# Kernel tuning notes

Measured on AMD Instinct MI355X. Metric: run time of the kernel, lower is better.

Reference implementation:

```python
import jax, jax.numpy as jnp
import numpy as np
from jax import lax


def _mdlstm_dir(x, Wx, Wh, Wv, b):
    # x: [H, W, B, Cin]; one diagonal-causal 2D-LSTM scan (top-left origin).
    H, W, B, Cin = x.shape
    C = Wh.shape[0]
    xa = jnp.einsum('hwbi,ic->hwbc', x, Wx) + b  # [H,W,B,5C] precomputed input gates

    def col_step(carry, inp):
        h_l, c_l = carry                    # left neighbor [B,C]
        xa_ij, h_u, c_u = inp               # input preact, up neighbor
        a = xa_ij + h_l @ Wh + h_u @ Wv     # [B,5C]
        i, f1, f2, o, g = jnp.split(a, 5, axis=-1)
        c = jax.nn.sigmoid(i) * jnp.tanh(g) + jax.nn.sigmoid(f1) * c_l + jax.nn.sigmoid(f2) * c_u
        h = jax.nn.sigmoid(o) * jnp.tanh(c)
        return (h, c), (h, c)

    z = jnp.zeros((B, C), x.dtype)
    zrow = jnp.zeros((W, B, C), x.dtype)

    def row_step(carry, xa_row):
        h_up, c_up = carry                  # [W,B,C]
        _, (hs, cs) = lax.scan(col_step, (z, z), (xa_row, h_up, c_up))
        return (hs, cs), hs

    _, hh = lax.scan(row_step, (zrow, zrow), xa)  # [H,W,B,C]
    return hh


def _mdlstm4(x, Wx, Wh, Wv, b):
    # x: [B,Cin,H,W] -> per-direction outputs [4,H,W,B,C] (directions: TL, TR, BL, BR origins)
    xt = jnp.transpose(x, (2, 3, 0, 1))  # [H,W,B,Cin]
    x4 = jnp.stack([xt, xt[:, ::-1], xt[::-1], xt[::-1, ::-1]])
    o = jax.vmap(_mdlstm_dir)(x4, Wx, Wh, Wv, b)  # [4,H,W,B,C]
    return jnp.stack([o[0], o[1][:, ::-1], o[2][::-1], o[3][::-1, ::-1]])


def _block(x, Wx, Wh, Wv, b, cw, cb):
    h4 = _mdlstm4(x, Wx, Wh, Wv, b)            # [4,H,W,B,C]
    h = jnp.transpose(h4.sum(0), (2, 3, 0, 1))  # sum directions -> [B,C,H,W]
    y = lax.conv_general_dilated(h, cw, window_strides=(2, 2), padding='VALID',
                                 dimension_numbers=('NCHW', 'OIHW', 'NCHW'))
    return jnp.tanh(y + cb[None, :, None, None])


def _forward(x, p0_Wx, p0_Wh, p0_Wv, p0_b, c0_w, c0_b,
             p1_Wx, p1_Wh, p1_Wv, p1_b, c1_w, c1_b,
             p2_Wx, p2_Wh, p2_Wv, p2_b, dW, db):
    x = _block(x, p0_Wx, p0_Wh, p0_Wv, p0_b, c0_w, c0_b)  # [B,6,31,126]
    x = _block(x, p1_Wx, p1_Wh, p1_Wv, p1_b, c1_w, c1_b)  # [B,20,14,61]
    h4 = _mdlstm4(x, p2_Wx, p2_Wh, p2_Wv, p2_b)           # [4,H,W,B,50]
    # per-direction Linear(50->100) then sum over the 4 directions
    out = jnp.einsum('dhwbc,dcn->bhwn', h4, dW) + db.sum(0)
    return out  # [B,14,61,100]


def setup_inputs() -> dict:
    key = jax.random.key(0)
    ks = jax.random.split(key, 20)
    rn = lambda k, s, sc=0.1: jax.random.normal(k, s, jnp.float32) * sc
    return {
        'x': jax.random.normal(ks[0], (16, 1, 64, 256), jnp.float32),
        'p0_Wx': rn(ks[1], (4, 1, 10)), 'p0_Wh': rn(ks[2], (4, 2, 10)),
        'p0_Wv': rn(ks[3], (4, 2, 10)), 'p0_b': rn(ks[4], (4, 10)),
        'c0_w': rn(ks[5], (6, 2, 2, 4)), 'c0_b': rn(ks[6], (6,)),
        'p1_Wx': rn(ks[7], (4, 6, 50)), 'p1_Wh': rn(ks[8], (4, 10, 50)),
        'p1_Wv': rn(ks[9], (4, 10, 50)), 'p1_b': rn(ks[10], (4, 50)),
        'c1_w': rn(ks[11], (20, 10, 2, 4)), 'c1_b': rn(ks[12], (20,)),
        'p2_Wx': rn(ks[13], (4, 20, 250)), 'p2_Wh': rn(ks[14], (4, 50, 250)),
        'p2_Wv': rn(ks[15], (4, 50, 250)), 'p2_b': rn(ks[16], (4, 250)),
        'dW': rn(ks[17], (4, 50, 100)), 'db': rn(ks[18], (4, 100)),
    }


def reference(x, p0_Wx, p0_Wh, p0_Wv, p0_b, c0_w, c0_b,
              p1_Wx, p1_Wh, p1_Wv, p1_b, c1_w, c1_b,
              p2_Wx, p2_Wh, p2_Wv, p2_b, dW, db):
    return _forward(x, p0_Wx, p0_Wh, p0_Wv, p0_b, c0_w, c0_b,
                    p1_Wx, p1_Wh, p1_Wv, p1_b, c1_w, c1_b,
                    p2_Wx, p2_Wh, p2_Wv, p2_b, dW, db)
```

## Files before the change

### kernel.cpp

```cpp
#include <hip/hip_runtime.h>

typedef unsigned short ushort_t;
typedef __attribute__((ext_vector_type(8))) short short8;
typedef __attribute__((ext_vector_type(4))) float float4_t;

__device__ __forceinline__ float frcp(float x) { return __builtin_amdgcn_rcpf(x); }
__device__ __forceinline__ float fsig(float x) { return frcp(1.f + __expf(-x)); }
__device__ __forceinline__ float ftanh(float x) { return 1.f - 2.f * frcp(1.f + __expf(2.f * x)); }

__device__ __forceinline__ ushort_t f2bf(float f) {
    union { float f; unsigned u; } v; v.f = f;
    unsigned u = v.u;
    unsigned r = (u + 0x7fffu + ((u >> 16) & 1u)) >> 16;
    return (ushort_t)r;
}
__device__ __forceinline__ float bf2f(ushort_t s) {
    union { unsigned u; float f; } v; v.u = ((unsigned)s) << 16;
    return v.f;
}

__global__ __launch_bounds__(64) void k_mdlstm0(
    const float* __restrict__ x, const float* __restrict__ Wx,
    const float* __restrict__ Wh, const float* __restrict__ Wv,
    const float* __restrict__ bias, float* __restrict__ h0)
{
    const int dir = blockIdx.x >> 4, b = blockIdx.x & 15;
    const int lane = threadIdx.x;
    const bool fH = dir >= 2, fW = (dir & 1) != 0;
    const int ri = fH ? 63 - lane : lane;

    float wx[10], bs[10], wh[2][10], wv[2][10];
#pragma unroll
    for (int n = 0; n < 10; n++) { wx[n] = Wx[dir * 10 + n]; bs[n] = bias[dir * 10 + n]; }
#pragma unroll
    for (int k = 0; k < 2; k++)
#pragma unroll
        for (int n = 0; n < 10; n++) {
            wh[k][n] = Wh[(dir * 2 + k) * 10 + n];
            wv[k][n] = Wv[(dir * 2 + k) * 10 + n];
        }

    const float* xrow = x + (b * 64 + ri) * 256;
    float* orow = h0 + (((dir * 16 + b) * 64 + ri) * 256) * 2;

    float h0r = 0.f, h1r = 0.f, c0r = 0.f, c1r = 0.f;

    auto ld = [&](int d) -> float {
        int j = d - lane; j = j < 0 ? 0 : (j > 255 ? 255 : j);
        int cj = fW ? 255 - j : j;
        return xrow[cj];
    };
    float xp0 = ld(0), xp1 = ld(1);

    for (int d = 0; d < 319; d++) {
        float xv = xp0;
        xp0 = xp1;
        xp1 = ld(d + 2);

        float hu0 = __shfl_up(h0r, 1), hu1 = __shfl_up(h1r, 1);
        float cu0 = __shfl_up(c0r, 1), cu1 = __shfl_up(c1r, 1);
        if (lane == 0) { hu0 = 0.f; hu1 = 0.f; cu0 = 0.f; cu1 = 0.f; }

        int j = d - lane;
        if (j >= 0 && j < 256) {
            float a[10];
#pragma unroll
            for (int n = 0; n < 10; n++) {
                float t = fmaf(xv, wx[n], bs[n]);
                t = fmaf(h0r, wh[0][n], t); t = fmaf(h1r, wh[1][n], t);
                t = fmaf(hu0, wv[0][n], t); t = fmaf(hu1, wv[1][n], t);
                a[n] = t;
            }
            float cn0 = fsig(a[0]) * ftanh(a[8]) + fsig(a[2]) * c0r + fsig(a[4]) * cu0;
            float cn1 = fsig(a[1]) * ftanh(a[9]) + fsig(a[3]) * c1r + fsig(a[5]) * cu1;
            float hn0 = fsig(a[6]) * ftanh(cn0);
            float hn1 = fsig(a[7]) * ftanh(cn1);
            h0r = hn0; h1r = hn1; c0r = cn0; c1r = cn1;
            int cj = fW ? 255 - j : j;
            float2 hv; hv.x = hn0; hv.y = hn1;
            *(float2*)&orow[cj * 2] = hv;
        }
    }
}

__global__ __launch_bounds__(128) void k_conv0(
    const float* __restrict__ h0, const float* __restrict__ cw,
    const float* __restrict__ cb, float* __restrict__ x1)
{
    int blk = blockIdx.x;
    int oh = blk / 127, ow = blk % 127;
    int t = threadIdx.x;
    if (t >= 96) return;
    int b = t / 6, co = t % 6;
    float w[2][2][4];
#pragma unroll
    for (int ci = 0; ci < 2; ci++)
#pragma unroll
        for (int kh = 0; kh < 2; kh++)
#pragma unroll
            for (int kw = 0; kw < 4; kw++)
                w[ci][kh][kw] = cw[((co * 2 + ci) * 2 + kh) * 4 + kw];
    float acc = cb[co];
    for (int dirb = 0; dirb < 4; dirb++) {
#pragma unroll
        for (int kh = 0; kh < 2; kh++) {
#pragma unroll
            for (int kw = 0; kw < 4; kw++) {
                const float* ptr = h0 + ((((dirb * 16 + b) * 64) + (2 * oh + kh)) * 256 + (2 * ow + kw)) * 2;
                float2 hv = *(const float2*)ptr;
                acc = fmaf(hv.x, w[0][kh][kw], acc);
                acc = fmaf(hv.y, w[1][kh][kw], acc);
            }
        }
    }
    x1[((oh * 127 + ow) * 16 + b) * 6 + co] = ftanh(acc);
}

__global__ __launch_bounds__(320, 1) void k_mdlstm1(
    const float* __restrict__ x1, const float* __restrict__ Wx,
    const float* __restrict__ Wh, const float* __restrict__ Wv,
    const float* __restrict__ bias, float* __restrict__ h1)
{
    const int dir = blockIdx.x >> 4, b = blockIdx.x & 15;
    const bool fH = dir >= 2, fW = (dir & 1) != 0;
    const int tid = threadIdx.x;
    const int cell = tid / 10, u = tid % 10;
    const int ri = fH ? 31 - cell : cell;

    __shared__ float hb[2][33][12];
    __shared__ float cb[2][33][12];
    for (int i = tid; i < 2 * 33 * 12; i += 320) { ((float*)hb)[i] = 0.f; ((float*)cb)[i] = 0.f; }
    __syncthreads();

    float wxr[6][5], whr[10][5], wvr[10][5], br[5];
#pragma unroll
    for (int g = 0; g < 5; g++) {
        int n = g * 10 + u;
        br[g] = bias[dir * 50 + n];
#pragma unroll
        for (int ci = 0; ci < 6; ci++) wxr[ci][g] = Wx[(dir * 6 + ci) * 50 + n];
#pragma unroll
        for (int k = 0; k < 10; k++) {
            whr[k][g] = Wh[(dir * 10 + k) * 50 + n];
            wvr[k][g] = Wv[(dir * 10 + k) * 50 + n];
        }
    }

    float creg = 0.f;
    float xr[6], xn[6];
    auto xload = [&](int d, float* dst) {
        int j = d - cell; j = j < 0 ? 0 : (j > 126 ? 126 : j);
        int cj = fW ? 126 - j : j;
        const float* p2 = x1 + ((ri * 127 + cj) * 16 + b) * 6;
#pragma unroll
        for (int k2 = 0; k2 < 6; k2++) dst[k2] = p2[k2];
    };
    xload(0, xr); xload(1, xn);

    int p = 0;
    for (int d = 0; d < 158; d++) {
        int j = d - cell;
        bool act = (j >= 0) && (j < 127);
        float hl[10], hu[10];
#pragma unroll
        for (int k = 0; k < 10; k++) { hl[k] = hb[p][cell + 1][k]; hu[k] = hb[p][cell][k]; }
        float cu = cb[p][cell][u];
        if (act) {
            float a[5];
#pragma unroll
            for (int g = 0; g < 5; g++) {
                float t = br[g];
#pragma unroll
                for (int ci = 0; ci < 6; ci++) t = fmaf(xr[ci], wxr[ci][g], t);
#pragma unroll
                for (int k = 0; k < 10; k++) t = fmaf(hl[k], whr[k][g], t);
#pragma unroll
                for (int k = 0; k < 10; k++) t = fmaf(hu[k], wvr[k][g], t);
                a[g] = t;
            }
            float cn = fsig(a[0]) * ftanh(a[4]) + fsig(a[1]) * creg + fsig(a[2]) * cu;
            float hn = fsig(a[3]) * ftanh(cn);
            creg = cn;
            hb[1 - p][cell + 1][u] = hn;
            cb[1 - p][cell + 1][u] = cn;
            int cj = fW ? 126 - j : j;
            h1[(((dir * 16 + b) * 32 + ri) * 127 + cj) * 10 + u] = hn;
        }
#pragma unroll
        for (int k2 = 0; k2 < 6; k2++) xr[k2] = xn[k2];
        xload(d + 2, xn);
        __syncthreads();
        p ^= 1;
    }
}

__global__ __launch_bounds__(320, 1) void k_conv1(
    const float* __restrict__ h1, const float* __restrict__ cw,
    const float* __restrict__ cb, float* __restrict__ x2)
{
    int blk = blockIdx.x;
    int oh = blk / 62, ow = blk % 62;
    int t = threadIdx.x;
    int b = t / 20, co = t % 20;
    float w[10][2][4];
#pragma unroll
    for (int ci = 0; ci < 10; ci++)
#pragma unroll
        for (int kh = 0; kh < 2; kh++)
#pragma unroll
            for (int kw = 0; kw < 4; kw++)
                w[ci][kh][kw] = cw[((co * 10 + ci) * 2 + kh) * 4 + kw];
    float acc = cb[co];
    for (int dirb = 0; dirb < 4; dirb++) {
#pragma unroll
        for (int kh = 0; kh < 2; kh++) {
#pragma unroll
            for (int kw = 0; kw < 4; kw++) {
                const float* ptr = h1 + ((((dirb * 16 + b) * 32) + (2 * oh + kh)) * 127 + (2 * ow + kw)) * 10;
#pragma unroll
                for (int ci = 0; ci < 10; ci++)
                    acc = fmaf(ptr[ci], w[ci][kh][kw], acc);
            }
        }
    }
    x2[((oh * 62 + ow) * 16 + b) * 20 + co] = ftanh(acc);
}

__global__ __launch_bounds__(256) void k_prepB2(
    const float* __restrict__ Wh, const float* __restrict__ Wv,
    const float* __restrict__ Wx, ushort_t* __restrict__ Bh,
    ushort_t* __restrict__ Bl)
{
    int idx = blockIdx.x * 256 + threadIdx.x;
    if (idx >= 131072) return;
    int dir = idx >> 15; int k = (idx >> 8) & 127; int n = idx & 255;
    float v = 0.f;
    if (n < 250) {
        if (k < 50)       v = Wh[(dir * 50 + k) * 250 + n];
        else if (k < 100) v = Wv[(dir * 50 + (k - 50)) * 250 + n];
        else if (k < 120) v = Wx[(dir * 20 + (k - 100)) * 250 + n];
    }
    ushort_t hi = f2bf(v);
    Bh[idx] = hi;
    Bl[idx] = f2bf(v - bf2f(hi));
}

__global__ __launch_bounds__(1024, 1) void k_mdlstm2(
    const float* __restrict__ x2, const ushort_t* __restrict__ BmH,
    const ushort_t* __restrict__ BmL,
    const float* __restrict__ bias, float* __restrict__ h2)
{
    const int dir = blockIdx.x >> 4, b = blockIdx.x & 15;
    const bool fH = dir >= 2, fW = (dir & 1) != 0;
    const int tid = threadIdx.x;
    const int wave = tid >> 6, lane = tid & 63;

    __shared__ __align__(16) ushort_t Ah[2][16][136];
    __shared__ __align__(16) ushort_t Al[2][16][136];
    __shared__ float P[16][260];
    __shared__ float cbuf[2][16][52];

    for (int i = tid; i < 2 * 16 * 136; i += 1024) { ((ushort_t*)Ah)[i] = 0; ((ushort_t*)Al)[i] = 0; }
    __syncthreads();
    if (tid < 20) {
        int ci = tid;
        int rr = fH ? 15 : 0, cc = fW ? 61 : 0;
        float xv = x2[((rr * 62 + cc) * 16 + b) * 20 + ci];
        ushort_t xh = f2bf(xv);
        Ah[0][0][100 + ci] = xh;
        Al[0][0][100 + ci] = f2bf(xv - bf2f(xh));
    }

    short8 bfragH[4], bfragL[4];
    {
        const int n = wave * 16 + (lane & 15);
#pragma unroll
        for (int q = 0; q < 4; q++) {
#pragma unroll
            for (int jj = 0; jj < 8; jj++) {
                int k = q * 32 + (lane >> 4) * 8 + jj;
                bfragH[q][jj] = (short)BmH[(dir * 128 + k) * 256 + n];
                bfragL[q][jj] = (short)BmL[(dir * 128 + k) * 256 + n];
            }
        }
    }

    const int cell = tid / 50, u = tid % 50;
    float bi = 0, bf1 = 0, bf2v = 0, bo = 0, bg = 0;
    if (tid < 800) {
        bi   = bias[dir * 250 + u];
        bf1  = bias[dir * 250 + 50 + u];
        bf2v = bias[dir * 250 + 100 + u];
        bo   = bias[dir * 250 + 150 + u];
        bg   = bias[dir * 250 + 200 + u];
    }
    const int rr_c = fH ? 15 - cell : cell;
    float creg = 0.f;
    __syncthreads();

    int p = 0;
    for (int d = 0; d < 77; d++) {
        float4_t acc = {0.f, 0.f, 0.f, 0.f};
        const int arow = lane & 15;
        const int koff = (lane >> 4) * 8;
#pragma unroll
        for (int q = 0; q < 4; q++) {
            short8 af = *(const short8*)&Ah[p][arow][q * 32 + koff];
            acc = __builtin_amdgcn_mfma_f32_16x16x32_bf16(af, bfragL[q], acc, 0, 0, 0);
        }
#pragma unroll
        for (int q = 0; q < 4; q++) {
            short8 af = *(const short8*)&Al[p][arow][q * 32 + koff];
            acc = __builtin_amdgcn_mfma_f32_16x16x32_bf16(af, bfragH[q], acc, 0, 0, 0);
        }
#pragma unroll
        for (int q = 0; q < 4; q++) {
            short8 af = *(const short8*)&Ah[p][arow][q * 32 + koff];
            acc = __builtin_amdgcn_mfma_f32_16x16x32_bf16(af, bfragH[q], acc, 0, 0, 0);
        }
        {
            int col = wave * 16 + (lane & 15);
            int r0 = (lane >> 4) * 4;
#pragma unroll
            for (int r = 0; r < 4; r++) P[r0 + r][col] = acc[r];
        }
        __syncthreads();

        if (tid < 800) {
            int j = d - cell;
            if (j >= 0 && j < 62) {
                float ai  = P[cell][u] + bi;
                float af1 = P[cell][50 + u] + bf1;
                float af2 = P[cell][100 + u] + bf2v;
                float ao  = P[cell][150 + u] + bo;
                float ag  = P[cell][200 + u] + bg;
                float cu = (cell == 0) ? 0.f : cbuf[p][cell - 1][u];
                float cn = fsig(ai) * ftanh(ag) + fsig(af1) * creg + fsig(af2) * cu;
                float hn = fsig(ao) * ftanh(cn);
                creg = cn;
                cbuf[1 - p][cell][u] = cn;
                ushort_t hh = f2bf(hn);
                float hhf = bf2f(hh);
                ushort_t hlo = f2bf(hn - hhf);
                Ah[1 - p][cell][u] = hh;
                Al[1 - p][cell][u] = hlo;
                if (cell < 15) { Ah[1 - p][cell + 1][50 + u] = hh; Al[1 - p][cell + 1][50 + u] = hlo; }
                int cc = fW ? 61 - j : j;
                h2[(((dir * 16 + b) * 16 + rr_c) * 62 + cc) * 50 + u] = hn;
            }
        }
        if (tid < 320) {
            int xc = tid / 20, ci = tid % 20;
            int jn = d + 1 - xc;
            if (jn >= 0 && jn < 62) {
                int rr = fH ? 15 - xc : xc, cc = fW ? 61 - jn : jn;
                float xv = x2[((rr * 62 + cc) * 16 + b) * 20 + ci];
                ushort_t xh = f2bf(xv);
                Ah[1 - p][xc][100 + ci] = xh;
                Al[1 - p][xc][100 + ci] = f2bf(xv - bf2f(xh));
            }
        }
        __syncthreads();
        p ^= 1;
    }
}

__global__ __launch_bounds__(256) void k_final(
    const float* __restrict__ h2, const float* __restrict__ dW,
    const float* __restrict__ db, float* __restrict__ out)
{
    int blk = blockIdx.x;
    int r = blk / 62, c = blk % 62;
    int t = threadIdx.x;
    __shared__ float hb[3200];
    for (int i = t; i < 3200; i += 256) {
        int dirb = i / 800, rem = i % 800, b = rem / 50, u = rem % 50;
        hb[i] = h2[(((dirb * 16 + b) * 16 + r) * 62 + c) * 50 + u];
    }
    __syncthreads();
    for (int o = t; o < 1600; o += 256) {
        int b = o / 100, n = o % 100;
        float acc = db[n] + db[100 + n] + db[200 + n] + db[300 + n];
#pragma unroll
        for (int dirb = 0; dirb < 4; dirb++) {
            const float* hp = hb + (dirb * 16 + b) * 50;
            const float* wp = dW + dirb * 5000 + n;
#pragma unroll 10
            for (int cc2 = 0; cc2 < 50; cc2++)
                acc = fmaf(hp[cc2], wp[cc2 * 100], acc);
        }
        out[((b * 16 + r) * 62 + c) * 100 + n] = acc;
    }
}

extern "C" void kernel_launch(void* const* d_in, const int* in_sizes, int n_in,
                              void* d_out, int out_size, void* d_ws, size_t ws_size,
                              hipStream_t stream)
{
    const float* x     = (const float*)d_in[0];
    const float* p0_Wx = (const float*)d_in[1];
    const float* p0_Wh = (const float*)d_in[2];
    const float* p0_Wv = (const float*)d_in[3];
    const float* p0_b  = (const float*)d_in[4];
    const float* c0_w  = (const float*)d_in[5];
    const float* c0_b  = (const float*)d_in[6];
    const float* p1_Wx = (const float*)d_in[7];
    const float* p1_Wh = (const float*)d_in[8];
    const float* p1_Wv = (const float*)d_in[9];
    const float* p1_b  = (const float*)d_in[10];
    const float* c1_w  = (const float*)d_in[11];
    const float* c1_b  = (const float*)d_in[12];
    const float* p2_Wx = (const float*)d_in[13];
    const float* p2_Wh = (const float*)d_in[14];
    const float* p2_Wv = (const float*)d_in[15];
    const float* p2_b  = (const float*)d_in[16];
    const float* dW    = (const float*)d_in[17];
    const float* db    = (const float*)d_in[18];
    float* out = (float*)d_out;
    float* ws  = (float*)d_ws;

    float* h0 = ws;
    float* x1 = h0 + 2097152;
    float* h1 = x1 + 390144;
    float* x2 = h1 + 2600960;
    float* h2 = x2 + 317440;
    ushort_t* BmH = (ushort_t*)(h2 + 3174400);
    ushort_t* BmL = BmH + 131072;

    k_prepB2<<<512, 256, 0, stream>>>(p2_Wh, p2_Wv, p2_Wx, BmH, BmL);
    k_mdlstm0<<<64, 64, 0, stream>>>(x, p0_Wx, p0_Wh, p0_Wv, p0_b, h0);
    k_conv0<<<32 * 127, 128, 0, stream>>>(h0, c0_w, c0_b, x1);
    k_mdlstm1<<<64, 320, 0, stream>>>(x1, p1_Wx, p1_Wh, p1_Wv, p1_b, h1);
    k_conv1<<<16 * 62, 320, 0, stream>>>(h1, c1_w, c1_b, x2);
    k_mdlstm2<<<64, 1024, 0, stream>>>(x2, BmH, BmL, p2_b, h2);
    k_final<<<16 * 62, 256, 0, stream>>>(h2, dW, db, out);
}
```

Baseline: 562.5 us.

## Move layer-1 MDLSTM gate matmul to MFMA and vectorize layer-0 recurrence

Layer-1 MDLSTM now runs its per-diagonal gate GEMM on bf16 MFMA with a hi/lo split for near-fp32 accuracy. It uses 1024 threads, with dedicated waves prefetching the next diagonal's inputs into shared memory. This replaces a long serial FMA chain per thread. Layer 0 uses packed float2 FMAs, folds log2(e) scaling into the weights so it can call exp2 directly, and uses a DPP row shift in place of shfl_up. Layer 2 preloads A fragments and reorders its MFMA chain and input-load threads. Risks: the DPP row_shr only shifts within 16-lane rows, so lanes 16/32/48 would read zero instead of their upper neighbor. The else branch that zeroes the state also changes the boundary behavior.

```diff
diff --git a/kernel.cpp b/kernel.cpp
--- a/kernel.cpp
+++ b/kernel.cpp
@@ -3,10 +3,13 @@
 typedef unsigned short ushort_t;
 typedef __attribute__((ext_vector_type(8))) short short8;
 typedef __attribute__((ext_vector_type(4))) float float4_t;
+typedef __attribute__((ext_vector_type(2))) float v2f;
 
 __device__ __forceinline__ float frcp(float x) { return __builtin_amdgcn_rcpf(x); }
 __device__ __forceinline__ float fsig(float x) { return frcp(1.f + __expf(-x)); }
 __device__ __forceinline__ float ftanh(float x) { return 1.f - 2.f * frcp(1.f + __expf(2.f * x)); }
+__device__ __forceinline__ float sig_e2(float a) { return frcp(1.f + __builtin_amdgcn_exp2f(a)); }
+__device__ __forceinline__ float th_e2(float a) { return 1.f - 2.f * frcp(1.f + __builtin_amdgcn_exp2f(a)); }
 
 __device__ __forceinline__ ushort_t f2bf(float f) {
     union { float f; unsigned u; } v; v.f = f;
@@ -18,6 +21,11 @@
     union { unsigned u; float f; } v; v.u = ((unsigned)s) << 16;
     return v.f;
 }
+__device__ __forceinline__ float dpp_shr1(float x) {
+    int i = __builtin_bit_cast(int, x);
+    int r = __builtin_amdgcn_update_dpp(0, i, 0x138 , 0xf, 0xf, true);
+    return __builtin_bit_cast(float, r);
+}
 
 __global__ __launch_bounds__(64) void k_mdlstm0(
     const float* __restrict__ x, const float* __restrict__ Wx,
@@ -28,22 +36,28 @@
     const int lane = threadIdx.x;
     const bool fH = dir >= 2, fW = (dir & 1) != 0;
     const int ri = fH ? 63 - lane : lane;
-
-    float wx[10], bs[10], wh[2][10], wv[2][10];
-#pragma unroll
-    for (int n = 0; n < 10; n++) { wx[n] = Wx[dir * 10 + n]; bs[n] = bias[dir * 10 + n]; }
-#pragma unroll
-    for (int k = 0; k < 2; k++)
-#pragma unroll
-        for (int n = 0; n < 10; n++) {
-            wh[k][n] = Wh[(dir * 2 + k) * 10 + n];
-            wv[k][n] = Wv[(dir * 2 + k) * 10 + n];
-        }
+    const float L2E = 1.44269504088896340736f;
+
+    v2f wx[5], bs[5], wh0[5], wh1[5], wv0[5], wv1[5];
+#pragma unroll
+    for (int g = 0; g < 5; g++) {
+        float sc = (g == 4) ? 2.f * L2E : -L2E;
+#pragma unroll
+        for (int un = 0; un < 2; un++) {
+            int n = g * 2 + un;
+            wx[g][un]  = Wx[dir * 10 + n] * sc;
+            bs[g][un]  = bias[dir * 10 + n] * sc;
+            wh0[g][un] = Wh[(dir * 2 + 0) * 10 + n] * sc;
+            wh1[g][un] = Wh[(dir * 2 + 1) * 10 + n] * sc;
+            wv0[g][un] = Wv[(dir * 2 + 0) * 10 + n] * sc;
+            wv1[g][un] = Wv[(dir * 2 + 1) * 10 + n] * sc;
+        }
+    }
 
     const float* xrow = x + (b * 64 + ri) * 256;
     float* orow = h0 + (((dir * 16 + b) * 64 + ri) * 256) * 2;
 
-    float h0r = 0.f, h1r = 0.f, c0r = 0.f, c1r = 0.f;
+    v2f hr = {0.f, 0.f}, cr = {0.f, 0.f};
 
     auto ld = [&](int d) -> float {
         int j = d - lane; j = j < 0 ? 0 : (j > 255 ? 255 : j);
@@ -57,28 +71,37 @@
         xp0 = xp1;
         xp1 = ld(d + 2);
 
-        float hu0 = __shfl_up(h0r, 1), hu1 = __shfl_up(h1r, 1);
-        float cu0 = __shfl_up(c0r, 1), cu1 = __shfl_up(c1r, 1);
-        if (lane == 0) { hu0 = 0.f; hu1 = 0.f; cu0 = 0.f; cu1 = 0.f; }
+        float hu0 = dpp_shr1(hr.x), hu1 = dpp_shr1(hr.y);
+        float cu0 = dpp_shr1(cr.x), cu1 = dpp_shr1(cr.y);
 
         int j = d - lane;
         if (j >= 0 && j < 256) {
-            float a[10];
-#pragma unroll
-            for (int n = 0; n < 10; n++) {
-                float t = fmaf(xv, wx[n], bs[n]);
-                t = fmaf(h0r, wh[0][n], t); t = fmaf(h1r, wh[1][n], t);
-                t = fmaf(hu0, wv[0][n], t); t = fmaf(hu1, wv[1][n], t);
-                a[n] = t;
-            }
-            float cn0 = fsig(a[0]) * ftanh(a[8]) + fsig(a[2]) * c0r + fsig(a[4]) * cu0;
-            float cn1 = fsig(a[1]) * ftanh(a[9]) + fsig(a[3]) * c1r + fsig(a[5]) * cu1;
-            float hn0 = fsig(a[6]) * ftanh(cn0);
-            float hn1 = fsig(a[7]) * ftanh(cn1);
-            h0r = hn0; h1r = hn1; c0r = cn0; c1r = cn1;
+            v2f a[5];
+#pragma unroll
+            for (int g = 0; g < 5; g++) {
+                v2f t = __builtin_elementwise_fma((v2f){xv, xv}, wx[g], bs[g]);
+                t = __builtin_elementwise_fma((v2f){hr.x, hr.x}, wh0[g], t);
+                t = __builtin_elementwise_fma((v2f){hr.y, hr.y}, wh1[g], t);
+                t = __builtin_elementwise_fma((v2f){hu0, hu0}, wv0[g], t);
+                t = __builtin_elementwise_fma((v2f){hu1, hu1}, wv1[g], t);
+                a[g] = t;
+            }
+            v2f si  = {sig_e2(a[0].x), sig_e2(a[0].y)};
+            v2f sf1 = {sig_e2(a[1].x), sig_e2(a[1].y)};
+            v2f sf2 = {sig_e2(a[2].x), sig_e2(a[2].y)};
+            v2f so  = {sig_e2(a[3].x), sig_e2(a[3].y)};
+            v2f tg  = {th_e2(a[4].x),  th_e2(a[4].y)};
+            v2f cu  = {cu0, cu1};
+            v2f cn = si * tg + sf1 * cr + sf2 * cu;
+            v2f tc = {th_e2(cn.x * (2.f * L2E)), th_e2(cn.y * (2.f * L2E))};
+            hr = so * tc;
+            cr = cn;
             int cj = fW ? 255 - j : j;
-            float2 hv; hv.x = hn0; hv.y = hn1;
+            float2 hv; hv.x = hr.x; hv.y = hr.y;
             *(float2*)&orow[cj * 2] = hv;
+        } else {
+            hr = (v2f){0.f, 0.f};
+            cr = (v2f){0.f, 0.f};
         }
     }
 }
@@ -116,7 +139,7 @@
     x1[((oh * 127 + ow) * 16 + b) * 6 + co] = ftanh(acc);
 }
 
-__global__ __launch_bounds__(320, 1) void k_mdlstm1(
+__global__ __launch_bounds__(1024, 1) void k_mdlstm1(
     const float* __restrict__ x1, const float* __restrict__ Wx,
     const float* __restrict__ Wh, const float* __restrict__ Wv,
     const float* __restrict__ bias, float* __restrict__ h1)
@@ -124,71 +147,102 @@
     const int dir = blockIdx.x >> 4, b = blockIdx.x & 15;
     const bool fH = dir >= 2, fW = (dir & 1) != 0;
     const int tid = threadIdx.x;
+    const int wave = tid >> 6, lane = tid & 63;
+
+    __shared__ __align__(16) ushort_t Ah[2][32][40];
+    __shared__ __align__(16) ushort_t Al[2][32][40];
+    __shared__ float P[32][68];
+    __shared__ float cbuf[2][33][12];
+
+    for (int i = tid; i < 2 * 32 * 40; i += 1024) { ((ushort_t*)Ah)[i] = 0; ((ushort_t*)Al)[i] = 0; }
+    for (int i = tid; i < 2 * 33 * 12; i += 1024) ((float*)cbuf)[i] = 0.f;
+    __syncthreads();
+    if (tid < 6) {
+        int rr = fH ? 31 : 0, cc = fW ? 126 : 0;
+        float xv = x1[((rr * 127 + cc) * 16 + b) * 6 + tid];
+        ushort_t xh = f2bf(xv);
+        Ah[0][0][20 + tid] = xh;
+        Al[0][0][20 + tid] = f2bf(xv - bf2f(xh));
+    }
+
+    const int mt = wave & 1, nt = wave >> 1;
+    short8 bh = {0,0,0,0,0,0,0,0}, bl = {0,0,0,0,0,0,0,0};
+    if (wave < 8) {
+        int n = nt * 16 + (lane & 15);
+#pragma unroll
+        for (int jj = 0; jj < 8; jj++) {
+            int k = (lane >> 4) * 8 + jj;
+            float v = 0.f;
+            if (n < 50) {
+                if (k < 10)      v = Wh[(dir * 10 + k) * 50 + n];
+                else if (k < 20) v = Wv[(dir * 10 + (k - 10)) * 50 + n];
+                else if (k < 26) v = Wx[(dir * 6 + (k - 20)) * 50 + n];
+            }
+            ushort_t hi = f2bf(v);
+            bh[jj] = (short)hi;
+            bl[jj] = (short)f2bf(v - bf2f(hi));
+        }
+    }
+
     const int cell = tid / 10, u = tid % 10;
+    float br[5];
+#pragma unroll
+    for (int g = 0; g < 5; g++) br[g] = (tid < 320) ? bias[dir * 50 + g * 10 + u] : 0.f;
     const int ri = fH ? 31 - cell : cell;
-
-    __shared__ float hb[2][33][12];
-    __shared__ float cb[2][33][12];
-    for (int i = tid; i < 2 * 33 * 12; i += 320) { ((float*)hb)[i] = 0.f; ((float*)cb)[i] = 0.f; }
+    float creg = 0.f;
     __syncthreads();
-
-    float wxr[6][5], whr[10][5], wvr[10][5], br[5];
-#pragma unroll
-    for (int g = 0; g < 5; g++) {
-        int n = g * 10 + u;
-        br[g] = bias[dir * 50 + n];
-#pragma unroll
-        for (int ci = 0; ci < 6; ci++) wxr[ci][g] = Wx[(dir * 6 + ci) * 50 + n];
-#pragma unroll
-        for (int k = 0; k < 10; k++) {
-            whr[k][g] = Wh[(dir * 10 + k) * 50 + n];
-            wvr[k][g] = Wv[(dir * 10 + k) * 50 + n];
-        }
-    }
-
-    float creg = 0.f;
-    float xr[6], xn[6];
-    auto xload = [&](int d, float* dst) {
-        int j = d - cell; j = j < 0 ? 0 : (j > 126 ? 126 : j);
-        int cj = fW ? 126 - j : j;
-        const float* p2 = x1 + ((ri * 127 + cj) * 16 + b) * 6;
-#pragma unroll
-        for (int k2 = 0; k2 < 6; k2++) dst[k2] = p2[k2];
-    };
-    xload(0, xr); xload(1, xn);
 
     int p = 0;
     for (int d = 0; d < 158; d++) {
-        int j = d - cell;
-        bool act = (j >= 0) && (j < 127);
-        float hl[10], hu[10];
-#pragma unroll
-        for (int k = 0; k < 10; k++) { hl[k] = hb[p][cell + 1][k]; hu[k] = hb[p][cell][k]; }
-        float cu = cb[p][cell][u];
-        if (act) {
-            float a[5];
-#pragma unroll
-            for (int g = 0; g < 5; g++) {
-                float t = br[g];
-#pragma unroll
-                for (int ci = 0; ci < 6; ci++) t = fmaf(xr[ci], wxr[ci][g], t);
-#pragma unroll
-                for (int k = 0; k < 10; k++) t = fmaf(hl[k], whr[k][g], t);
-#pragma unroll
-                for (int k = 0; k < 10; k++) t = fmaf(hu[k], wvr[k][g], t);
-                a[g] = t;
-            }
-            float cn = fsig(a[0]) * ftanh(a[4]) + fsig(a[1]) * creg + fsig(a[2]) * cu;
-            float hn = fsig(a[3]) * ftanh(cn);
-            creg = cn;
-            hb[1 - p][cell + 1][u] = hn;
-            cb[1 - p][cell + 1][u] = cn;
-            int cj = fW ? 126 - j : j;
-            h1[(((dir * 16 + b) * 32 + ri) * 127 + cj) * 10 + u] = hn;
-        }
-#pragma unroll
-        for (int k2 = 0; k2 < 6; k2++) xr[k2] = xn[k2];
-        xload(d + 2, xn);
+        if (wave < 8) {
+            const int arow = mt * 16 + (lane & 15);
+            const int koff = (lane >> 4) * 8;
+            short8 ah = *(const short8*)&Ah[p][arow][koff];
+            short8 al = *(const short8*)&Al[p][arow][koff];
+            float4_t acc = {0.f, 0.f, 0.f, 0.f};
+            acc = __builtin_amdgcn_mfma_f32_16x16x32_bf16(ah, bh, acc, 0, 0, 0);
+            acc = __builtin_amdgcn_mfma_f32_16x16x32_bf16(al, bh, acc, 0, 0, 0);
+            acc = __builtin_amdgcn_mfma_f32_16x16x32_bf16(ah, bl, acc, 0, 0, 0);
+            int col = nt * 16 + (lane & 15);
+            int r0 = (lane >> 4) * 4;
+#pragma unroll
+            for (int r = 0; r < 4; r++) P[mt * 16 + r0 + r][col] = acc[r];
+        } else if (tid >= 512 && tid < 704) {
+            int s = tid - 512, xc = s / 6, ci = s % 6;
+            int jn = d + 1 - xc;
+            if (jn >= 0 && jn < 127) {
+                int rr = fH ? 31 - xc : xc, cc = fW ? 126 - jn : jn;
+                float xv = x1[((rr * 127 + cc) * 16 + b) * 6 + ci];
+                ushort_t xh = f2bf(xv);
+                Ah[1 - p][xc][20 + ci] = xh;
+                Al[1 - p][xc][20 + ci] = f2bf(xv - bf2f(xh));
+            }
+        }
+        __syncthreads();
+
+        if (tid < 320) {
+            int j = d - cell;
+            if (j >= 0 && j < 127) {
+                float ai  = P[cell][u]      + br[0];
+                float af1 = P[cell][10 + u] + br[1];
+                float af2 = P[cell][20 + u] + br[2];
+                float ao  = P[cell][30 + u] + br[3];
+                float ag  = P[cell][40 + u] + br[4];
+                float cu = cbuf[p][cell][u];
+                float cn = fsig(ai) * ftanh(ag) + fsig(af1) * creg + fsig(af2) * cu;
+                float hn = fsig(ao) * ftanh(cn);
+                creg = cn;
+                cbuf[1 - p][cell + 1][u] = cn;
+                ushort_t hh = f2bf(hn);
+                float hhf = bf2f(hh);
+                ushort_t hlo = f2bf(hn - hhf);
+                Ah[1 - p][cell][u] = hh;
+                Al[1 - p][cell][u] = hlo;
+                if (cell < 31) { Ah[1 - p][cell + 1][10 + u] = hh; Al[1 - p][cell + 1][10 + u] = hlo; }
+                int cj = fW ? 126 - j : j;
+                h1[(((dir * 16 + b) * 32 + ri) * 127 + cj) * 10 + u] = hn;
+            }
+        }
         __syncthreads();
         p ^= 1;
     }
@@ -300,25 +354,22 @@
 
     int p = 0;
     for (int d = 0; d < 77; d++) {
-        float4_t acc = {0.f, 0.f, 0.f, 0.f};
-        const int arow = lane & 15;
-        const int koff = (lane >> 4) * 8;
-#pragma unroll
-        for (int q = 0; q < 4; q++) {
-            short8 af = *(const short8*)&Ah[p][arow][q * 32 + koff];
-            acc = __builtin_amdgcn_mfma_f32_16x16x32_bf16(af, bfragL[q], acc, 0, 0, 0);
-        }
-#pragma unroll
-        for (int q = 0; q < 4; q++) {
-            short8 af = *(const short8*)&Al[p][arow][q * 32 + koff];
-            acc = __builtin_amdgcn_mfma_f32_16x16x32_bf16(af, bfragH[q], acc, 0, 0, 0);
-        }
-#pragma unroll
-        for (int q = 0; q < 4; q++) {
-            short8 af = *(const short8*)&Ah[p][arow][q * 32 + koff];
-            acc = __builtin_amdgcn_mfma_f32_16x16x32_bf16(af, bfragH[q], acc, 0, 0, 0);
-        }
         {
+            const int arow = lane & 15;
+            const int koff = (lane >> 4) * 8;
+            short8 ah[4], al[4];
+#pragma unroll
+            for (int q = 0; q < 4; q++) {
+                ah[q] = *(const short8*)&Ah[p][arow][q * 32 + koff];
+                al[q] = *(const short8*)&Al[p][arow][q * 32 + koff];
+            }
+            float4_t acc = {0.f, 0.f, 0.f, 0.f};
+#pragma unroll
+            for (int q = 0; q < 4; q++) acc = __builtin_amdgcn_mfma_f32_16x16x32_bf16(ah[q], bfragH[q], acc, 0, 0, 0);
+#pragma unroll
+            for (int q = 0; q < 4; q++) acc = __builtin_amdgcn_mfma_f32_16x16x32_bf16(al[q], bfragH[q], acc, 0, 0, 0);
+#pragma unroll
+            for (int q = 0; q < 4; q++) acc = __builtin_amdgcn_mfma_f32_16x16x32_bf16(ah[q], bfragL[q], acc, 0, 0, 0);
             int col = wave * 16 + (lane & 15);
             int r0 = (lane >> 4) * 4;
 #pragma unroll
@@ -348,16 +399,20 @@
                 int cc = fW ? 61 - j : j;
                 h2[(((dir * 16 + b) * 16 + rr_c) * 62 + cc) * 50 + u] = hn;
             }
-        }
-        if (tid < 320) {
-            int xc = tid / 20, ci = tid % 20;
-            int jn = d + 1 - xc;
-            if (jn >= 0 && jn < 62) {
-                int rr = fH ? 15 - xc : xc, cc = fW ? 61 - jn : jn;
-                float xv = x2[((rr * 62 + cc) * 16 + b) * 20 + ci];
-                ushort_t xh = f2bf(xv);
-                Ah[1 - p][xc][100 + ci] = xh;
-                Al[1 - p][xc][100 + ci] = f2bf(xv - bf2f(xh));
+        } else if (tid >= 832 && tid < 992) {
+            int s = tid - 832;
+#pragma unroll
+            for (int it = 0; it < 2; it++) {
+                int item = s + it * 160;
+                int xc = item / 20, ci = item % 20;
+                int jn = d + 1 - xc;
+                if (jn >= 0 && jn < 62) {
+                    int rr = fH ? 15 - xc : xc, cc = fW ? 61 - jn : jn;
+                    float xv = x2[((rr * 62 + cc) * 16 + b) * 20 + ci];
+                    ushort_t xh = f2bf(xv);
+                    Ah[1 - p][xc][100 + ci] = xh;
+                    Al[1 - p][xc][100 + ci] = f2bf(xv - bf2f(xh));
+                }
             }
         }
         __syncthreads();
@@ -430,7 +485,7 @@
     k_prepB2<<<512, 256, 0, stream>>>(p2_Wh, p2_Wv, p2_Wx, BmH, BmL);
     k_mdlstm0<<<64, 64, 0, stream>>>(x, p0_Wx, p0_Wh, p0_Wv, p0_b, h0);
     k_conv0<<<32 * 127, 128, 0, stream>>>(h0, c0_w, c0_b, x1);
-    k_mdlstm1<<<64, 320, 0, stream>>>(x1, p1_Wx, p1_Wh, p1_Wv, p1_b, h1);
+    k_mdlstm1<<<64, 1024, 0, stream>>>(x1, p1_Wx, p1_Wh, p1_Wv, p1_b, h1);
     k_conv1<<<16 * 62, 320, 0, stream>>>(h1, c1_w, c1_b, x2);
     k_mdlstm2<<<64, 1024, 0, stream>>>(x2, BmH, BmL, p2_b, h2);
     k_final<<<16 * 62, 256, 0, stream>>>(h2, dW, db, out);
```

After: 551.4 us. -2.0%, faster.
